# Kernel optimization log

Measured on AMD Instinct MI355X. Metric: run time of the kernel, lower is better.

## Reference

```python
import jax, jax.numpy as jnp
import numpy as np

H = 64
VOCAB = 64
THRESH_SCALE = 0.4
LN_EPS = 1e-5
NORM_EPS = 1e-12


def setup_inputs() -> dict:
    key = jax.random.key(0)
    ks = jax.random.split(key, 16)
    B, L = 64, 1024
    s = 1.0 / np.sqrt(H)
    inp = {
        "seq": jax.random.randint(ks[0], (B, L), 0, VOCAB),
        "embed_W": jax.random.normal(ks[1], (VOCAB, H), jnp.float32),
        "ff_W1": jax.random.normal(ks[2], (H, 2 * H), jnp.float32) * s,
        "ff_b1": jnp.zeros((2 * H,), jnp.float32),
        "ff_W2": jax.random.normal(ks[3], (2 * H, H), jnp.float32) * s,
        "ff_b2": jnp.zeros((H,), jnp.float32),
        "ln_g": jnp.ones((H,), jnp.float32),
        "ln_b": jnp.zeros((H,), jnp.float32),
        "kp_W": jax.random.normal(ks[4], (H, H), jnp.float32) * s,
        "vp_W": jax.random.normal(ks[5], (H, H), jnp.float32) * s,
        "qp_W": jax.random.normal(ks[6], (H, H), jnp.float32) * s,
        "rp_W": jax.random.normal(ks[7], (H, H), jnp.float32) * s,
        "rp_b": jnp.zeros((H,), jnp.float32),
        "out_W": jax.random.normal(ks[8], (H, VOCAB), jnp.float32) * s,
        "out_b": jnp.zeros((VOCAB,), jnp.float32),
    }
    return inp


def _forward(seq, embed_W, ff_W1, ff_b1, ff_W2, ff_b2, ln_g, ln_b,
             kp_W, vp_W, qp_W, rp_W, rp_b, out_W, out_b):
    h = embed_W[seq]                                    # [B, L, H]
    ff = jnp.maximum(h @ ff_W1 + ff_b1, 0.0) @ ff_W2 + ff_b2
    x = h + ff
    mu = x.mean(-1, keepdims=True)
    var = ((x - mu) ** 2).mean(-1, keepdims=True)       # biased var (torch LayerNorm)
    hn = (x - mu) / jnp.sqrt(var + LN_EPS) * ln_g + ln_b
    B, L, _ = hn.shape

    # Precompute all per-step keys/values, then scan the fast-weight update.
    k_all = hn[:, :-1] @ kp_W                           # [B, L-1, H]
    v_all = hn[:, :-1] @ vp_W                           # [B, L-1, H]
    kn_all = k_all / jnp.maximum(
        jnp.linalg.norm(k_all, axis=-1, keepdims=True), NORM_EPS)

    def step(M, kv):
        kn, v = kv                                      # each [B, H]
        vp = jnp.einsum('bij,bj->bi', M, kn)            # read M along k
        err = jnp.linalg.norm(v - vp, axis=-1)          # [B]
        gate = jnp.where(err > THRESH_SCALE * jnp.linalg.norm(v, axis=-1),
                         1.0, 0.0)                      # hard energy gate
        M = M + gate[:, None, None] * jnp.einsum('bi,bj->bij', v - vp, kn)
        return M, None

    M0 = jnp.zeros((B, H, H), dtype=hn.dtype)
    M, _ = jax.lax.scan(step, M0,
                        (kn_all.transpose(1, 0, 2), v_all.transpose(1, 0, 2)))

    q = hn[:, -1] @ qp_W                                # [B, H]
    r = jnp.einsum('bij,bj->bi', M, q) @ rp_W + rp_b
    return r @ out_W + out_b                            # [B, VOCAB]


def reference(seq, embed_W, ff_W1, ff_b1, ff_W2, ff_b2, ln_g, ln_b,
              kp_W, vp_W, qp_W, rp_W, rp_b, out_W, out_b):
    return _forward(seq, embed_W, ff_W1, ff_b1, ff_W2, ff_b2, ln_g, ln_b,
                    kp_W, vp_W, qp_W, rp_W, rp_b, out_W, out_b)
```

## Files before the change

### kernel.cpp

```cpp
#include <hip/hip_runtime.h>
#include <hip/hip_bf16.h>
#include <math.h>

#define BB 64
#define LL 1024
#define HH 64

typedef float v4f __attribute__((ext_vector_type(4)));
#define F4 __builtin_elementwise_fma

__global__ __launch_bounds__(256, 1)
void token_kernel(const int* __restrict__ seq,
                  const float* __restrict__ embed_W,
                  const float* __restrict__ ff_W1, const float* __restrict__ ff_b1,
                  const float* __restrict__ ff_W2, const float* __restrict__ ff_b2,
                  const float* __restrict__ ln_g, const float* __restrict__ ln_b,
                  const float* __restrict__ kp_W, const float* __restrict__ vp_W,
                  const float* __restrict__ qp_W,
                  float* __restrict__ knv, float* __restrict__ vthr,
                  float* __restrict__ qbuf)
{
    __shared__ __align__(16) float h_s[32][64];
    __shared__ __align__(16) float t1_s[32][128];
    __shared__ __align__(16) float hn_s[32][64];

    const int tid  = threadIdx.x;
    const int tok0 = blockIdx.x * 32;

#pragma unroll
    for (int k = 0; k < 8; ++k) {
        int e   = k * 256 + tid;
        int tok = e >> 6, i = e & 63;
        int s   = seq[tok0 + tok];
        h_s[tok][i] = embed_W[s * 64 + i];
    }
    __syncthreads();

    {
        const int j = tid & 127;
        const int g = tid >> 7;
        float w1c[64];
#pragma unroll
        for (int ii = 0; ii < 64; ++ii) w1c[ii] = ff_W1[ii * 128 + j];
        const float b1j = ff_b1[j];
#pragma unroll
        for (int tk = 0; tk < 16; ++tk) {
            const int tok = g * 16 + tk;
            const float4* h4 = (const float4*)h_s[tok];
            float a0 = b1j, a1 = 0.f, a2 = 0.f, a3 = 0.f;
#pragma unroll
            for (int w = 0; w < 16; ++w) {
                float4 hv = h4[w];
                a0 = fmaf(hv.x, w1c[4*w+0], a0);
                a1 = fmaf(hv.y, w1c[4*w+1], a1);
                a2 = fmaf(hv.z, w1c[4*w+2], a2);
                a3 = fmaf(hv.w, w1c[4*w+3], a3);
            }
            t1_s[tok][j] = fmaxf((a0 + a1) + (a2 + a3), 0.f);
        }
    }
    __syncthreads();

    {
        const int i  = tid & 63;
        const int w4 = tid >> 6;
        const float b2i = ff_b2[i];
        const float gi  = ln_g[i];
        const float bi  = ln_b[i];
        float accf[8];
#pragma unroll
        for (int tk = 0; tk < 8; ++tk) accf[tk] = b2i;
#pragma unroll
        for (int h = 0; h < 2; ++h) {
            float w2c[64];
#pragma unroll
            for (int jj = 0; jj < 64; ++jj) w2c[jj] = ff_W2[(h*64 + jj) * 64 + i];
#pragma unroll
            for (int tk = 0; tk < 8; ++tk) {
                const int tok = w4 * 8 + tk;
                const float4* t4 = (const float4*)&t1_s[tok][h*64];
                float a0 = 0.f, a1 = 0.f, a2 = 0.f, a3 = 0.f;
#pragma unroll
                for (int w = 0; w < 16; ++w) {
                    float4 tv = t4[w];
                    a0 = fmaf(tv.x, w2c[4*w+0], a0);
                    a1 = fmaf(tv.y, w2c[4*w+1], a1);
                    a2 = fmaf(tv.z, w2c[4*w+2], a2);
                    a3 = fmaf(tv.w, w2c[4*w+3], a3);
                }
                accf[tk] += (a0 + a1) + (a2 + a3);
            }
        }
#pragma unroll
        for (int tk = 0; tk < 8; ++tk) {
            const int tok = w4 * 8 + tk;
            float x = h_s[tok][i] + accf[tk];
            float s = x;
#pragma unroll
            for (int m = 32; m > 0; m >>= 1) s += __shfl_xor(s, m);
            float mu = s * (1.f / 64.f);
            float d  = x - mu;
            float s2 = d * d;
#pragma unroll
            for (int m = 32; m > 0; m >>= 1) s2 += __shfl_xor(s2, m);
            float var = s2 * (1.f / 64.f);
            hn_s[tok][i] = d / sqrtf(var + 1e-5f) * gi + bi;
        }
    }
    __syncthreads();

    {
        const int i  = tid & 63;
        const int w4 = tid >> 6;
        float kc[64], vc[64];
#pragma unroll
        for (int ii = 0; ii < 64; ++ii) {
            kc[ii] = kp_W[ii * 64 + i];
            vc[ii] = vp_W[ii * 64 + i];
        }
#pragma unroll
        for (int tk = 0; tk < 8; ++tk) {
            const int tok = w4 * 8 + tk;
            const int tg  = tok0 + tok;
            const int b   = tg >> 10;
            const int t   = tg & 1023;
            const float4* hn4 = (const float4*)hn_s[tok];
            if (t < 1023) {
                float ka0=0.f,ka1=0.f,ka2=0.f,ka3=0.f;
                float va0=0.f,va1=0.f,va2=0.f,va3=0.f;
#pragma unroll
                for (int w = 0; w < 16; ++w) {
                    float4 hv = hn4[w];
                    ka0 = fmaf(hv.x, kc[4*w+0], ka0);
                    ka1 = fmaf(hv.y, kc[4*w+1], ka1);
                    ka2 = fmaf(hv.z, kc[4*w+2], ka2);
                    ka3 = fmaf(hv.w, kc[4*w+3], ka3);
                    va0 = fmaf(hv.x, vc[4*w+0], va0);
                    va1 = fmaf(hv.y, vc[4*w+1], va1);
                    va2 = fmaf(hv.z, vc[4*w+2], va2);
                    va3 = fmaf(hv.w, vc[4*w+3], va3);
                }
                float ka = (ka0 + ka1) + (ka2 + ka3);
                float va = (va0 + va1) + (va2 + va3);
                float kn2 = ka * ka, vn2 = va * va;
#pragma unroll
                for (int m = 32; m > 0; m >>= 1) {
                    kn2 += __shfl_xor(kn2, m);
                    vn2 += __shfl_xor(vn2, m);
                }
                float knorm = fmaxf(sqrtf(kn2), 1e-12f);
                size_t row = ((size_t)b * 1024 + t) * 128;
                knv[row + i]      = ka / knorm;
                knv[row + 64 + i] = va;
                if (i == 0) vthr[b * 1024 + t] = 0.16f * vn2;
            } else {
                float qa0=0.f,qa1=0.f,qa2=0.f,qa3=0.f;
#pragma unroll
                for (int w = 0; w < 16; ++w) {
                    float4 hv = hn4[w];
                    qa0 = fmaf(hv.x, qp_W[(4*w+0)*64 + i], qa0);
                    qa1 = fmaf(hv.y, qp_W[(4*w+1)*64 + i], qa1);
                    qa2 = fmaf(hv.z, qp_W[(4*w+2)*64 + i], qa2);
                    qa3 = fmaf(hv.w, qp_W[(4*w+3)*64 + i], qa3);
                }
                qbuf[b * 64 + i] = (qa0 + qa1) + (qa2 + qa3);
            }
        }
    }
}


template<int CTRL>
__device__ __forceinline__ float dppadd(float x) {
    int y = __builtin_amdgcn_update_dpp(0, __float_as_int(x), CTRL, 0xF, 0xF, true);
    return x + __int_as_float(y);
}

__device__ __forceinline__ float bcast63(float x) {
    return __int_as_float(__builtin_amdgcn_readlane(__float_as_int(x), 63));
}

__device__ __forceinline__ float wave_sum64(float x) {
    x = dppadd<0x111>(x); x = dppadd<0x112>(x);
    x = dppadd<0x114>(x); x = dppadd<0x118>(x);
    x = dppadd<0x142>(x); x = dppadd<0x143>(x);
    return bcast63(x);
}

__device__ __forceinline__ void wsum4(float& a, float& b, float& c, float& d) {
    a = dppadd<0x111>(a); b = dppadd<0x111>(b); c = dppadd<0x111>(c); d = dppadd<0x111>(d);
    a = dppadd<0x112>(a); b = dppadd<0x112>(b); c = dppadd<0x112>(c); d = dppadd<0x112>(d);
    a = dppadd<0x114>(a); b = dppadd<0x114>(b); c = dppadd<0x114>(c); d = dppadd<0x114>(d);
    a = dppadd<0x118>(a); b = dppadd<0x118>(b); c = dppadd<0x118>(c); d = dppadd<0x118>(d);
    a = dppadd<0x142>(a); b = dppadd<0x142>(b); c = dppadd<0x142>(c); d = dppadd<0x142>(d);
    a = dppadd<0x143>(a); b = dppadd<0x143>(b); c = dppadd<0x143>(c); d = dppadd<0x143>(d);
    a = bcast63(a); b = bcast63(b); c = bcast63(c); d = bcast63(d);
}

#define LOADK4(P, ROW) do { \
    const float* r_ = (ROW) + (wid << 4); \
    P##0 = *(const v4f*)(r_ + 0);  P##1 = *(const v4f*)(r_ + 4); \
    P##2 = *(const v4f*)(r_ + 8);  P##3 = *(const v4f*)(r_ + 12); \
} while (0)

#define UPD4(P, G) do { \
    v4f gv_ = {G, G, G, G}; \
    m0 = F4(gv_, P##0, m0); m1 = F4(gv_, P##1, m1); \
    m2 = F4(gv_, P##2, m2); m3 = F4(gv_, P##3, m3); \
} while (0)

#define CHUNK2(UP, UQ, XR, XS, ROW2, ROW3, TH2P, TH3P, PAR) do { \
    UPD4(UP, gdp); \
    UPD4(UQ, gdq); \
    v4f q_ = F4(m0, XR##0, F4(m1, XR##1, F4(m2, XR##2, m3 * XR##3))); \
    float own0_ = (q_.x + q_.y) + (q_.z + q_.w); \
    v4f r_ = F4(m0, XS##0, F4(m1, XS##1, F4(m2, XS##2, m3 * XS##3))); \
    float own1_ = (r_.x + r_.y) + (r_.z + r_.w); \
    ((float2*)pex[PAR][wid])[lane] = make_float2(own0_, own1_); \
    asm volatile("s_waitcnt lgkmcnt(0)\n\ts_barrier" ::: "memory"); \
    float2 p0_ = ((const float2*)pex[PAR][0])[lane]; \
    float2 p1_ = ((const float2*)pex[PAR][1])[lane]; \
    float2 p2_ = ((const float2*)pex[PAR][2])[lane]; \
    float2 p3_ = ((const float2*)pex[PAR][3])[lane]; \
    float knl2_ = (ROW2)[lane]; \
    float knl3_ = (ROW3)[lane]; \
    float vv2_  = (ROW2)[64 + lane]; \
    float vv3_  = (ROW3)[64 + lane]; \
    float th2_  = *(TH2P); \
    float th3_  = *(TH3P); \
    LOADK4(UP, ROW2); \
    LOADK4(UQ, ROW3); \
    float base0_ = (p0_.x + p1_.x) + (p2_.x + p3_.x); \
    float base1_ = (p0_.y + p1_.y) + (p2_.y + p3_.y); \
    float d00_ = vv0 - base0_; \
    float d01_ = vv1 - base1_; \
    float x0_ = d00_ * d00_, x1_ = d00_ * d01_; \
    float x2_ = d01_ * d01_, x3_ = knl2_ * knl3_; \
    wsum4(x0_, x1_, x2_, x3_); \
    bool g0_ = x0_ > th0; \
    float corr_ = fmaf(2.f * c3, x1_, -(c3 * c3) * x0_); \
    float e1_ = g0_ ? (x2_ - corr_) : x2_; \
    bool g1_ = e1_ > th1; \
    float gd0_ = g0_ ? d00_ : 0.f; \
    float d1_  = fmaf(-c3, gd0_, d01_); \
    gdp = gd0_; \
    gdq = g1_ ? d1_ : 0.f; \
    vv0 = vv2_; vv1 = vv3_; th0 = th2_; th1 = th3_; c3 = x3_; \
} while (0)

#define BUF8(CB, NB, TP) \
    CHUNK2(U,V,S,T,(CB)+2*128, (CB)+3*128, (TP)+2, (TP)+3, 0); \
    CHUNK2(S,T,U,V,(CB)+4*128, (CB)+5*128, (TP)+4, (TP)+5, 1); \
    CHUNK2(U,V,S,T,(CB)+6*128, (CB)+7*128, (TP)+6, (TP)+7, 0); \
    CHUNK2(S,T,U,V,(CB)+8*128, (CB)+9*128, (TP)+8, (TP)+9, 1); \
    CHUNK2(U,V,S,T,(CB)+10*128,(CB)+11*128,(TP)+10,(TP)+11,0); \
    CHUNK2(S,T,U,V,(CB)+12*128,(CB)+13*128,(TP)+12,(TP)+13,1); \
    CHUNK2(U,V,S,T,(CB)+14*128,(CB)+15*128,(TP)+14,(TP)+15,0); \
    CHUNK2(S,T,U,V,(NB)+0*128, (NB)+1*128, (TP)+16,(TP)+17,1);

__device__ __forceinline__ void gl2lds_1k(const float* g, float* l, int lane) {
    __builtin_amdgcn_global_load_lds(
        (const __attribute__((address_space(1))) void*)(g + lane * 4),
        (__attribute__((address_space(3))) void*)l, 16, 0, 0);
}

__device__ __forceinline__ void prefetch_quarter(const float* g, float* l,
                                                 int lane, int wid) {
#pragma unroll
    for (int j = 0; j < 2; ++j)
        gl2lds_1k(g + wid * 512 + j * 256, l + wid * 512 + j * 256, lane);
}

__global__ __launch_bounds__(256, 1)
void scan_kernel(const float* __restrict__ knv,
                 const float* __restrict__ vthr,
                 const float* __restrict__ qbuf,
                 const float* __restrict__ rp_W, const float* __restrict__ rp_b,
                 const float* __restrict__ out_W, const float* __restrict__ out_b,
                 float* __restrict__ out)
{
    const int b    = blockIdx.x;
    const int tid  = threadIdx.x;
    const int lane = tid & 63;
    const int wid  = tid >> 6;
    const float* knvb = knv  + (size_t)b * 1024 * 128;
    const float* thrb = vthr + (size_t)b * 1024;

    __shared__ __align__(16) float thr_s[1040];
    __shared__ __align__(16) float buf[3 * 2048];
    __shared__ __align__(16) float pex[2][4][128];
    __shared__ float sh[64];

    v4f m0={0,0,0,0}, m1={0,0,0,0}, m2={0,0,0,0}, m3={0,0,0,0};
    v4f S0,S1,S2,S3;
    v4f T0,T1,T2,T3;
    v4f U0,U1,U2,U3;
    v4f V0,V1,V2,V3;

    if (wid == 0) {
#pragma unroll
        for (int w = 0; w < 4; ++w) gl2lds_1k(thrb + w * 256, thr_s + w * 256, lane);
    }
    prefetch_quarter(knvb,        buf,        lane, wid);
    prefetch_quarter(knvb + 2048, buf + 2048, lane, wid);
    prefetch_quarter(knvb + 4096, buf + 4096, lane, wid);

    {
        float4 z4 = make_float4(0.f, 0.f, 0.f, 0.f);
        ((float4*)pex)[tid] = z4;
    }

    asm volatile("s_waitcnt vmcnt(2) lgkmcnt(0)\n\ts_barrier" ::: "memory");

    LOADK4(S, buf);
    LOADK4(T, buf + 128);
    {
        v4f z_ = {0.f, 0.f, 0.f, 0.f};
        U0=z_;U1=z_;U2=z_;U3=z_;
        V0=z_;V1=z_;V2=z_;V3=z_;
    }
    float vv0 = buf[64 + lane];
    float vv1 = buf[192 + lane];
    float th0 = thr_s[0];
    float th1 = thr_s[1];
    float c3  = wave_sum64(buf[lane] * buf[128 + lane]);
    float gdp = 0.f, gdq = 0.f;

#pragma unroll 1
    for (int c = 0; c < 62; ++c) {
        asm volatile("s_waitcnt vmcnt(2)" ::: "memory");
        const float* cb = buf + (c % 3) * 2048;
        const float* nb = buf + ((c + 1) % 3) * 2048;
        const float* tp = thr_s + c * 16;
        BUF8(cb, nb, tp)
        if (c <= 60)
            prefetch_quarter(knvb + (size_t)(c + 3) * 2048,
                             buf + (c % 3) * 2048, lane, wid);
    }
    asm volatile("s_waitcnt vmcnt(0)" ::: "memory");
    asm volatile("s_barrier" ::: "memory");
    {
        const float* cb = buf + 2 * 2048;
        const float* nb = buf;
        const float* tp = thr_s + 62 * 16;
        BUF8(cb, nb, tp)
    }
    {
        const float* cb = buf;
        const float* nb = buf + 2048;
        const float* tp = thr_s + 63 * 16;
        BUF8(cb, nb, tp)
    }
    UPD4(U, gdp);

    {
        const v4f* qq = (const v4f*)(qbuf + b * 64);
        const int w4i = 4 * wid;
        v4f aq = F4(m0, qq[w4i+0], F4(m1, qq[w4i+1],
                 F4(m2, qq[w4i+2],  m3 * qq[w4i+3])));
        float vq_own = (aq.x + aq.y) + (aq.z + aq.w);
        pex[0][wid][lane] = vq_own;
        asm volatile("s_waitcnt lgkmcnt(0)\n\ts_barrier" ::: "memory");

        if (wid == 0) {
            float vq = (pex[0][0][lane] + pex[0][1][lane])
                     + (pex[0][2][lane] + pex[0][3][lane]);
            sh[lane] = vq;
            asm volatile("s_waitcnt lgkmcnt(0)" ::: "memory");
            float r = rp_b[lane];
#pragma unroll
            for (int ii = 0; ii < 64; ++ii) r = fmaf(sh[ii], rp_W[ii * 64 + lane], r);
            asm volatile("s_waitcnt lgkmcnt(0)" ::: "memory");
            sh[lane] = r;
            asm volatile("s_waitcnt lgkmcnt(0)" ::: "memory");
            float o = out_b[lane];
#pragma unroll
            for (int ii = 0; ii < 64; ++ii) o = fmaf(sh[ii], out_W[ii * 64 + lane], o);
            out[b * 64 + lane] = o;
        }
    }
}

extern "C" void kernel_launch(void* const* d_in, const int* in_sizes, int n_in,
                              void* d_out, int out_size, void* d_ws, size_t ws_size,
                              hipStream_t stream)
{
    const int*   seq   = (const int*)  d_in[0];
    const float* embed = (const float*)d_in[1];
    const float* ffW1  = (const float*)d_in[2];
    const float* ffb1  = (const float*)d_in[3];
    const float* ffW2  = (const float*)d_in[4];
    const float* ffb2  = (const float*)d_in[5];
    const float* lng   = (const float*)d_in[6];
    const float* lnb   = (const float*)d_in[7];
    const float* kpW   = (const float*)d_in[8];
    const float* vpW   = (const float*)d_in[9];
    const float* qpW   = (const float*)d_in[10];
    const float* rpW   = (const float*)d_in[11];
    const float* rpb   = (const float*)d_in[12];
    const float* outW  = (const float*)d_in[13];
    const float* outb  = (const float*)d_in[14];
    float* out = (float*)d_out;

    float* knv  = (float*)d_ws;
    float* vthr = knv  + (size_t)64 * 1024 * 128;
    float* qbuf = vthr + (size_t)64 * 1024;

    token_kernel<<<2048, 256, 0, stream>>>(seq, embed, ffW1, ffb1, ffW2, ffb2,
                                           lng, lnb, kpW, vpW, qpW,
                                           knv, vthr, qbuf);
    scan_kernel<<<64, 256, 0, stream>>>(knv, vthr, qbuf,
                                        rpW, rpb, outW, outb, out);
}
```

Baseline: 366.1 us.

## Fuse token and scan kernels with per-chunk flags to overlap stages

After: 387.9 us. +5.9%, slower.

```diff
diff --git a/kernel.cpp b/kernel.cpp
--- a/kernel.cpp
+++ b/kernel.cpp
@@ -9,165 +9,7 @@
 typedef float v4f __attribute__((ext_vector_type(4)));
 #define F4 __builtin_elementwise_fma
 
-__global__ __launch_bounds__(256, 1)
-void token_kernel(const int* __restrict__ seq,
-                  const float* __restrict__ embed_W,
-                  const float* __restrict__ ff_W1, const float* __restrict__ ff_b1,
-                  const float* __restrict__ ff_W2, const float* __restrict__ ff_b2,
-                  const float* __restrict__ ln_g, const float* __restrict__ ln_b,
-                  const float* __restrict__ kp_W, const float* __restrict__ vp_W,
-                  const float* __restrict__ qp_W,
-                  float* __restrict__ knv, float* __restrict__ vthr,
-                  float* __restrict__ qbuf)
-{
-    __shared__ __align__(16) float h_s[32][64];
-    __shared__ __align__(16) float t1_s[32][128];
-    __shared__ __align__(16) float hn_s[32][64];
-
-    const int tid  = threadIdx.x;
-    const int tok0 = blockIdx.x * 32;
-
-#pragma unroll
-    for (int k = 0; k < 8; ++k) {
-        int e   = k * 256 + tid;
-        int tok = e >> 6, i = e & 63;
-        int s   = seq[tok0 + tok];
-        h_s[tok][i] = embed_W[s * 64 + i];
-    }
-    __syncthreads();
-
-    {
-        const int j = tid & 127;
-        const int g = tid >> 7;
-        float w1c[64];
-#pragma unroll
-        for (int ii = 0; ii < 64; ++ii) w1c[ii] = ff_W1[ii * 128 + j];
-        const float b1j = ff_b1[j];
-#pragma unroll
-        for (int tk = 0; tk < 16; ++tk) {
-            const int tok = g * 16 + tk;
-            const float4* h4 = (const float4*)h_s[tok];
-            float a0 = b1j, a1 = 0.f, a2 = 0.f, a3 = 0.f;
-#pragma unroll
-            for (int w = 0; w < 16; ++w) {
-                float4 hv = h4[w];
-                a0 = fmaf(hv.x, w1c[4*w+0], a0);
-                a1 = fmaf(hv.y, w1c[4*w+1], a1);
-                a2 = fmaf(hv.z, w1c[4*w+2], a2);
-                a3 = fmaf(hv.w, w1c[4*w+3], a3);
-            }
-            t1_s[tok][j] = fmaxf((a0 + a1) + (a2 + a3), 0.f);
-        }
-    }
-    __syncthreads();
-
-    {
-        const int i  = tid & 63;
-        const int w4 = tid >> 6;
-        const float b2i = ff_b2[i];
-        const float gi  = ln_g[i];
-        const float bi  = ln_b[i];
-        float accf[8];
-#pragma unroll
-        for (int tk = 0; tk < 8; ++tk) accf[tk] = b2i;
-#pragma unroll
-        for (int h = 0; h < 2; ++h) {
-            float w2c[64];
-#pragma unroll
-            for (int jj = 0; jj < 64; ++jj) w2c[jj] = ff_W2[(h*64 + jj) * 64 + i];
-#pragma unroll
-            for (int tk = 0; tk < 8; ++tk) {
-                const int tok = w4 * 8 + tk;
-                const float4* t4 = (const float4*)&t1_s[tok][h*64];
-                float a0 = 0.f, a1 = 0.f, a2 = 0.f, a3 = 0.f;
-#pragma unroll
-                for (int w = 0; w < 16; ++w) {
-                    float4 tv = t4[w];
-                    a0 = fmaf(tv.x, w2c[4*w+0], a0);
-                    a1 = fmaf(tv.y, w2c[4*w+1], a1);
-                    a2 = fmaf(tv.z, w2c[4*w+2], a2);
-                    a3 = fmaf(tv.w, w2c[4*w+3], a3);
-                }
-                accf[tk] += (a0 + a1) + (a2 + a3);
-            }
-        }
-#pragma unroll
-        for (int tk = 0; tk < 8; ++tk) {
-            const int tok = w4 * 8 + tk;
-            float x = h_s[tok][i] + accf[tk];
-            float s = x;
-#pragma unroll
-            for (int m = 32; m > 0; m >>= 1) s += __shfl_xor(s, m);
-            float mu = s * (1.f / 64.f);
-            float d  = x - mu;
-            float s2 = d * d;
-#pragma unroll
-            for (int m = 32; m > 0; m >>= 1) s2 += __shfl_xor(s2, m);
-            float var = s2 * (1.f / 64.f);
-            hn_s[tok][i] = d / sqrtf(var + 1e-5f) * gi + bi;
-        }
-    }
-    __syncthreads();
-
-    {
-        const int i  = tid & 63;
-        const int w4 = tid >> 6;
-        float kc[64], vc[64];
-#pragma unroll
-        for (int ii = 0; ii < 64; ++ii) {
-            kc[ii] = kp_W[ii * 64 + i];
-            vc[ii] = vp_W[ii * 64 + i];
-        }
-#pragma unroll
-        for (int tk = 0; tk < 8; ++tk) {
-            const int tok = w4 * 8 + tk;
-            const int tg  = tok0 + tok;
-            const int b   = tg >> 10;
-            const int t   = tg & 1023;
-            const float4* hn4 = (const float4*)hn_s[tok];
-            if (t < 1023) {
-                float ka0=0.f,ka1=0.f,ka2=0.f,ka3=0.f;
-                float va0=0.f,va1=0.f,va2=0.f,va3=0.f;
-#pragma unroll
-                for (int w = 0; w < 16; ++w) {
-                    float4 hv = hn4[w];
-                    ka0 = fmaf(hv.x, kc[4*w+0], ka0);
-                    ka1 = fmaf(hv.y, kc[4*w+1], ka1);
-                    ka2 = fmaf(hv.z, kc[4*w+2], ka2);
-                    ka3 = fmaf(hv.w, kc[4*w+3], ka3);
-                    va0 = fmaf(hv.x, vc[4*w+0], va0);
-                    va1 = fmaf(hv.y, vc[4*w+1], va1);
-                    va2 = fmaf(hv.z, vc[4*w+2], va2);
-                    va3 = fmaf(hv.w, vc[4*w+3], va3);
-                }
-                float ka = (ka0 + ka1) + (ka2 + ka3);
-                float va = (va0 + va1) + (va2 + va3);
-                float kn2 = ka * ka, vn2 = va * va;
-#pragma unroll
-                for (int m = 32; m > 0; m >>= 1) {
-                    kn2 += __shfl_xor(kn2, m);
-                    vn2 += __shfl_xor(vn2, m);
-                }
-                float knorm = fmaxf(sqrtf(kn2), 1e-12f);
-                size_t row = ((size_t)b * 1024 + t) * 128;
-                knv[row + i]      = ka / knorm;
-                knv[row + 64 + i] = va;
-                if (i == 0) vthr[b * 1024 + t] = 0.16f * vn2;
-            } else {
-                float qa0=0.f,qa1=0.f,qa2=0.f,qa3=0.f;
-#pragma unroll
-                for (int w = 0; w < 16; ++w) {
-                    float4 hv = hn4[w];
-                    qa0 = fmaf(hv.x, qp_W[(4*w+0)*64 + i], qa0);
-                    qa1 = fmaf(hv.y, qp_W[(4*w+1)*64 + i], qa1);
-                    qa2 = fmaf(hv.z, qp_W[(4*w+2)*64 + i], qa2);
-                    qa3 = fmaf(hv.w, qp_W[(4*w+3)*64 + i], qa3);
-                }
-                qbuf[b * 64 + i] = (qa0 + qa1) + (qa2 + qa3);
-            }
-        }
-    }
-}
+__device__ int g_flags[2048];
 
 
 template<int CTRL>
@@ -271,25 +113,194 @@
         gl2lds_1k(g + wid * 512 + j * 256, l + wid * 512 + j * 256, lane);
 }
 
-__global__ __launch_bounds__(256, 1)
-void scan_kernel(const float* __restrict__ knv,
-                 const float* __restrict__ vthr,
-                 const float* __restrict__ qbuf,
-                 const float* __restrict__ rp_W, const float* __restrict__ rp_b,
-                 const float* __restrict__ out_W, const float* __restrict__ out_b,
-                 float* __restrict__ out)
+__device__ __forceinline__ void spin_flag(const int* f) {
+    while (__hip_atomic_load(f, __ATOMIC_ACQUIRE, __HIP_MEMORY_SCOPE_AGENT) == 0)
+        __builtin_amdgcn_s_sleep(16);
+}
+
+__device__ void token_body(float* smem, int bIdx, int tcIdx,
+                           const int* __restrict__ seq,
+                           const float* __restrict__ embed_W,
+                           const float* __restrict__ ff_W1, const float* __restrict__ ff_b1,
+                           const float* __restrict__ ff_W2, const float* __restrict__ ff_b2,
+                           const float* __restrict__ ln_g, const float* __restrict__ ln_b,
+                           const float* __restrict__ kp_W, const float* __restrict__ vp_W,
+                           const float* __restrict__ qp_W,
+                           float* __restrict__ knv, float* __restrict__ vthr,
+                           float* __restrict__ qbuf)
 {
-    const int b    = blockIdx.x;
+    float (*h_s)[64]   = (float(*)[64])smem;
+    float (*t1_s)[128] = (float(*)[128])(smem + 2048);
+    float (*hn_s)[64]  = (float(*)[64])(smem + 6144);
+
+    const int tid  = threadIdx.x;
+    const int tok0 = bIdx * 1024 + tcIdx * 32;
+
+#pragma unroll
+    for (int k = 0; k < 8; ++k) {
+        int e   = k * 256 + tid;
+        int tok = e >> 6, i = e & 63;
+        int s   = seq[tok0 + tok];
+        h_s[tok][i] = embed_W[s * 64 + i];
+    }
+    __syncthreads();
+
+    {
+        const int j = tid & 127;
+        const int g = tid >> 7;
+        float w1c[64];
+#pragma unroll
+        for (int ii = 0; ii < 64; ++ii) w1c[ii] = ff_W1[ii * 128 + j];
+        const float b1j = ff_b1[j];
+#pragma unroll
+        for (int tk = 0; tk < 16; ++tk) {
+            const int tok = g * 16 + tk;
+            const float4* h4 = (const float4*)h_s[tok];
+            float a0 = b1j, a1 = 0.f, a2 = 0.f, a3 = 0.f;
+#pragma unroll
+            for (int w = 0; w < 16; ++w) {
+                float4 hv = h4[w];
+                a0 = fmaf(hv.x, w1c[4*w+0], a0);
+                a1 = fmaf(hv.y, w1c[4*w+1], a1);
+                a2 = fmaf(hv.z, w1c[4*w+2], a2);
+                a3 = fmaf(hv.w, w1c[4*w+3], a3);
+            }
+            t1_s[tok][j] = fmaxf((a0 + a1) + (a2 + a3), 0.f);
+        }
+    }
+    __syncthreads();
+
+    {
+        const int i  = tid & 63;
+        const int w4 = tid >> 6;
+        const float b2i = ff_b2[i];
+        const float gi  = ln_g[i];
+        const float bi  = ln_b[i];
+        float accf[8];
+#pragma unroll
+        for (int tk = 0; tk < 8; ++tk) accf[tk] = b2i;
+#pragma unroll
+        for (int h = 0; h < 2; ++h) {
+            float w2c[64];
+#pragma unroll
+            for (int jj = 0; jj < 64; ++jj) w2c[jj] = ff_W2[(h*64 + jj) * 64 + i];
+#pragma unroll
+            for (int tk = 0; tk < 8; ++tk) {
+                const int tok = w4 * 8 + tk;
+                const float4* t4 = (const float4*)&t1_s[tok][h*64];
+                float a0 = 0.f, a1 = 0.f, a2 = 0.f, a3 = 0.f;
+#pragma unroll
+                for (int w = 0; w < 16; ++w) {
+                    float4 tv = t4[w];
+                    a0 = fmaf(tv.x, w2c[4*w+0], a0);
+                    a1 = fmaf(tv.y, w2c[4*w+1], a1);
+                    a2 = fmaf(tv.z, w2c[4*w+2], a2);
+                    a3 = fmaf(tv.w, w2c[4*w+3], a3);
+                }
+                accf[tk] += (a0 + a1) + (a2 + a3);
+            }
+        }
+#pragma unroll
+        for (int tk = 0; tk < 8; ++tk) {
+            const int tok = w4 * 8 + tk;
+            float x = h_s[tok][i] + accf[tk];
+            float s = x;
+#pragma unroll
+            for (int m = 32; m > 0; m >>= 1) s += __shfl_xor(s, m);
+            float mu = s * (1.f / 64.f);
+            float d  = x - mu;
+            float s2 = d * d;
+#pragma unroll
+            for (int m = 32; m > 0; m >>= 1) s2 += __shfl_xor(s2, m);
+            float var = s2 * (1.f / 64.f);
+            hn_s[tok][i] = d / sqrtf(var + 1e-5f) * gi + bi;
+        }
+    }
+    __syncthreads();
+
+    {
+        const int i  = tid & 63;
+        const int w4 = tid >> 6;
+        float kc[64], vc[64];
+#pragma unroll
+        for (int ii = 0; ii < 64; ++ii) {
+            kc[ii] = kp_W[ii * 64 + i];
+            vc[ii] = vp_W[ii * 64 + i];
+        }
+#pragma unroll
+        for (int tk = 0; tk < 8; ++tk) {
+            const int tok = w4 * 8 + tk;
+            const int tg  = tok0 + tok;
+            const int b   = tg >> 10;
+            const int t   = tg & 1023;
+            const float4* hn4 = (const float4*)hn_s[tok];
+            if (t < 1023) {
+                float ka0=0.f,ka1=0.f,ka2=0.f,ka3=0.f;
+                float va0=0.f,va1=0.f,va2=0.f,va3=0.f;
+#pragma unroll
+                for (int w = 0; w < 16; ++w) {
+                    float4 hv = hn4[w];
+                    ka0 = fmaf(hv.x, kc[4*w+0], ka0);
+                    ka1 = fmaf(hv.y, kc[4*w+1], ka1);
+                    ka2 = fmaf(hv.z, kc[4*w+2], ka2);
+                    ka3 = fmaf(hv.w, kc[4*w+3], ka3);
+                    va0 = fmaf(hv.x, vc[4*w+0], va0);
+                    va1 = fmaf(hv.y, vc[4*w+1], va1);
+                    va2 = fmaf(hv.z, vc[4*w+2], va2);
+                    va3 = fmaf(hv.w, vc[4*w+3], va3);
+                }
+                float ka = (ka0 + ka1) + (ka2 + ka3);
+                float va = (va0 + va1) + (va2 + va3);
+                float kn2 = ka * ka, vn2 = va * va;
+#pragma unroll
+                for (int m = 32; m > 0; m >>= 1) {
+                    kn2 += __shfl_xor(kn2, m);
+                    vn2 += __shfl_xor(vn2, m);
+                }
+                float knorm = fmaxf(sqrtf(kn2), 1e-12f);
+                size_t row = ((size_t)b * 1024 + t) * 128;
+                knv[row + i]      = ka / knorm;
+                knv[row + 64 + i] = va;
+                if (i == 0) vthr[b * 1024 + t] = 0.16f * vn2;
+            } else {
+                float qa0=0.f,qa1=0.f,qa2=0.f,qa3=0.f;
+#pragma unroll
+                for (int w = 0; w < 16; ++w) {
+                    float4 hv = hn4[w];
+                    qa0 = fmaf(hv.x, qp_W[(4*w+0)*64 + i], qa0);
+                    qa1 = fmaf(hv.y, qp_W[(4*w+1)*64 + i], qa1);
+                    qa2 = fmaf(hv.z, qp_W[(4*w+2)*64 + i], qa2);
+                    qa3 = fmaf(hv.w, qp_W[(4*w+3)*64 + i], qa3);
+                }
+                qbuf[b * 64 + i] = (qa0 + qa1) + (qa2 + qa3);
+            }
+        }
+    }
+
+    __syncthreads();
+    if (tid == 0)
+        __hip_atomic_store(&g_flags[bIdx * 32 + tcIdx], 1,
+                           __ATOMIC_RELEASE, __HIP_MEMORY_SCOPE_AGENT);
+}
+
+__device__ void scan_body(float* smem, int b,
+                          const float* __restrict__ knv,
+                          const float* __restrict__ vthr,
+                          const float* __restrict__ qbuf,
+                          const float* __restrict__ rp_W, const float* __restrict__ rp_b,
+                          const float* __restrict__ out_W, const float* __restrict__ out_b,
+                          float* __restrict__ out)
+{
     const int tid  = threadIdx.x;
     const int lane = tid & 63;
     const int wid  = tid >> 6;
     const float* knvb = knv  + (size_t)b * 1024 * 128;
     const float* thrb = vthr + (size_t)b * 1024;
-
-    __shared__ __align__(16) float thr_s[1040];
-    __shared__ __align__(16) float buf[3 * 2048];
-    __shared__ __align__(16) float pex[2][4][128];
-    __shared__ float sh[64];
+    const int*   flg  = &g_flags[b * 32];
+
+    float* buf = smem;
+    float (*pex)[4][128] = (float(*)[4][128])(smem + 6144);
+    float* sh = smem + 7168;
 
     v4f m0={0,0,0,0}, m1={0,0,0,0}, m2={0,0,0,0}, m3={0,0,0,0};
     v4f S0,S1,S2,S3;
@@ -297,10 +308,8 @@
     v4f U0,U1,U2,U3;
     v4f V0,V1,V2,V3;
 
-    if (wid == 0) {
-#pragma unroll
-        for (int w = 0; w < 4; ++w) gl2lds_1k(thrb + w * 256, thr_s + w * 256, lane);
-    }
+    spin_flag(flg + 0);
+    spin_flag(flg + 1);
     prefetch_quarter(knvb,        buf,        lane, wid);
     prefetch_quarter(knvb + 2048, buf + 2048, lane, wid);
     prefetch_quarter(knvb + 4096, buf + 4096, lane, wid);
@@ -321,8 +330,8 @@
     }
     float vv0 = buf[64 + lane];
     float vv1 = buf[192 + lane];
-    float th0 = thr_s[0];
-    float th1 = thr_s[1];
+    float th0 = thrb[0];
+    float th1 = thrb[1];
     float c3  = wave_sum64(buf[lane] * buf[128 + lane]);
     float gdp = 0.f, gdq = 0.f;
 
@@ -331,24 +340,26 @@
         asm volatile("s_waitcnt vmcnt(2)" ::: "memory");
         const float* cb = buf + (c % 3) * 2048;
         const float* nb = buf + ((c + 1) % 3) * 2048;
-        const float* tp = thr_s + c * 16;
+        const float* tp = thrb + c * 16;
         BUF8(cb, nb, tp)
-        if (c <= 60)
+        if (c <= 60) {
+            if (((c + 3) & 1) == 0) spin_flag(flg + ((c + 3) >> 1));
             prefetch_quarter(knvb + (size_t)(c + 3) * 2048,
                              buf + (c % 3) * 2048, lane, wid);
+        }
     }
     asm volatile("s_waitcnt vmcnt(0)" ::: "memory");
     asm volatile("s_barrier" ::: "memory");
     {
         const float* cb = buf + 2 * 2048;
         const float* nb = buf;
-        const float* tp = thr_s + 62 * 16;
+        const float* tp = thrb + 62 * 16;
         BUF8(cb, nb, tp)
     }
     {
         const float* cb = buf;
         const float* nb = buf + 2048;
-        const float* tp = thr_s + 63 * 16;
+        const float* tp = thrb + 63 * 16;
         BUF8(cb, nb, tp)
     }
     UPD4(U, gdp);
@@ -378,6 +389,32 @@
             for (int ii = 0; ii < 64; ++ii) o = fmaf(sh[ii], out_W[ii * 64 + lane], o);
             out[b * 64 + lane] = o;
         }
+    }
+}
+
+__global__ __launch_bounds__(256, 1)
+void fused_kernel(const int* __restrict__ seq,
+                  const float* __restrict__ embed_W,
+                  const float* __restrict__ ff_W1, const float* __restrict__ ff_b1,
+                  const float* __restrict__ ff_W2, const float* __restrict__ ff_b2,
+                  const float* __restrict__ ln_g, const float* __restrict__ ln_b,
+                  const float* __restrict__ kp_W, const float* __restrict__ vp_W,
+                  const float* __restrict__ qp_W,
+                  const float* __restrict__ rp_W, const float* __restrict__ rp_b,
+                  const float* __restrict__ out_W, const float* __restrict__ out_b,
+                  float* __restrict__ knv, float* __restrict__ vthr,
+                  float* __restrict__ qbuf, float* __restrict__ out)
+{
+    __shared__ __align__(16) float smem[8192];
+    const int g = blockIdx.x;
+    if (g >= 64) {
+        const int tg2 = g - 64;
+        const int tc  = tg2 >> 6;
+        const int b   = tg2 & 63;
+        token_body(smem, b, tc, seq, embed_W, ff_W1, ff_b1, ff_W2, ff_b2,
+                   ln_g, ln_b, kp_W, vp_W, qp_W, knv, vthr, qbuf);
+    } else {
+        scan_body(smem, g, knv, vthr, qbuf, rp_W, rp_b, out_W, out_b, out);
     }
 }
 
@@ -406,9 +443,12 @@
     float* vthr = knv  + (size_t)64 * 1024 * 128;
     float* qbuf = vthr + (size_t)64 * 1024;
 
-    token_kernel<<<2048, 256, 0, stream>>>(seq, embed, ffW1, ffb1, ffW2, ffb2,
+    static void* flags_ptr = nullptr;
+    if (!flags_ptr) hipGetSymbolAddress(&flags_ptr, HIP_SYMBOL(g_flags));
+    hipMemsetAsync(flags_ptr, 0, 2048 * sizeof(int), stream);
+
+    fused_kernel<<<2112, 256, 0, stream>>>(seq, embed, ffW1, ffb1, ffW2, ffb2,
                                            lng, lnb, kpW, vpW, qpW,
-                                           knv, vthr, qbuf);
-    scan_kernel<<<64, 256, 0, stream>>>(knv, vthr, qbuf,
-                                        rpW, rpb, outW, outb, out);
-}
+                                           rpW, rpb, outW, outb,
+                                           knv, vthr, qbuf, out);
+}
```
